# Kernel optimization log

Hardware: AMD Instinct MI355X
Metric: run time of the kernel (lower is better)

The kernel has to match this reference:

```python
import jax, jax.numpy as jnp
import numpy as np
from jax import lax

H, HH = 512, 256          # hidden_size, per-direction TLSTM hidden
B, S = 16, 4096
NOTE_V, CHUNK_V = 512, 512
NUM_LABELS = 1
STD = 0.02                # initializer_range
LN_EPS = 1e-12


def setup_inputs() -> dict:
    key = jax.random.key(0)
    ks = jax.random.split(key, 12)
    n = lambda k, s: jax.random.normal(k, s, jnp.float32) * STD
    return {
        "inputs": jax.random.normal(ks[0], (B, S, H), jnp.float32),
        "times": jax.random.uniform(ks[1], (B, S, 1), jnp.float32),
        "new_note_ids": jax.random.randint(ks[2], (B, S), 0, NOTE_V),
        "new_chunk_ids": jax.random.randint(ks[3], (B, S), 0, CHUNK_V),
        "note_emb": n(ks[4], (NOTE_V, H)),
        "chunk_emb": n(ks[5], (CHUNK_V, H)),
        "W_comb": n(ks[6], (3 * H, H)),
        "b_comb": jnp.zeros((H,), jnp.float32),
        "ln_g": jnp.ones((H,), jnp.float32),
        "ln_b": jnp.zeros((H,), jnp.float32),
        "Wx": n(ks[7], (2, 4, H, HH)),    # [dir, gate(i,f,o,c), in, hid]
        "Wh": n(ks[8], (2, 4, HH, HH)),
        "bg": jnp.zeros((2, 4, HH), jnp.float32),
        "Wd": n(ks[9], (2, HH, HH)),      # W_decomp per direction
        "bd": jnp.zeros((2, HH), jnp.float32),
        "W_cls": n(ks[10], (H, NUM_LABELS)),
        "b_cls": jnp.zeros((NUM_LABELS,), jnp.float32),
    }


def _run_dir(xseq, tseq, Wx, Wh, bg, Wd, bd):
    # xseq: [S,B,H], tseq: [S,B,1]
    def step(carry, xt):
        h, c = carry
        x, t = xt
        T = 1.0 / jnp.log(t + jnp.e)                  # time decay, [B,1] -> broadcast [B,HH]
        c_st = jnp.tanh(c @ Wd + bd)                  # short-term memory
        c_adj = c - c_st + T * c_st                   # discounted cell
        g = jax.nn.sigmoid(jnp.einsum('bd,kdh->kbh', x, Wx)
                           + jnp.einsum('bh,kho->kbo', h, Wh)
                           + bg[:, None, :])          # note: candidate uses sigmoid in original
        i, f, o, cg = g[0], g[1], g[2], g[3]
        ct = f * c_adj + i * cg
        hn = o * jnp.tanh(ct)
        return (hn, ct), hn
    z = jnp.zeros((xseq.shape[1], Wh.shape[-1]), xseq.dtype)
    _, hs = lax.scan(step, (z, z), (xseq, tseq))
    return hs  # [S,B,HH]


def reference(inputs, times, new_note_ids, new_chunk_ids, note_emb, chunk_emb,
              W_comb, b_comb, ln_g, ln_b, Wx, Wh, bg, Wd, bd, W_cls, b_cls):
    # PatientLevelEmbedding (embed_mode='all'), dropout = identity (eval)
    x = jnp.concatenate([inputs, note_emb[new_note_ids], chunk_emb[new_chunk_ids]],
                        axis=-1) @ W_comb + b_comb
    mu = jnp.mean(x, -1, keepdims=True)
    var = jnp.mean((x - mu) ** 2, -1, keepdims=True)
    x = (x - mu) / jnp.sqrt(var + LN_EPS) * ln_g + ln_b

    xs = jnp.transpose(x, (1, 0, 2))      # [S,B,H]  (batch_first permute)
    ts = jnp.transpose(times, (1, 0, 2))  # [S,B,1]

    hs_f = _run_dir(xs, ts, Wx[0], Wh[0], bg[0], Wd[0], bd[0])
    # backward pass: time at step 0 is times[0], then flipped times shifted by one
    t_bwd = jnp.concatenate([ts[:1], jnp.flip(ts, 0)[:-1]], axis=0)
    hs_b = _run_dir(jnp.flip(xs, 0), t_bwd, Wx[1], Wh[1], bg[1], Wd[1], bd[1])

    hidden = jnp.concatenate([hs_f, hs_b], axis=-1)   # [S,B,2*HH]
    drop_in = hidden[-1, 0, :]                        # == lstm_output[0, -1, :] batch-first
    logits = drop_in @ W_cls + b_cls
    logits = jnp.where(jnp.isnan(logits) | jnp.isinf(logits), 0.0, logits)
    pred = jax.nn.sigmoid(logits)
    pred = jnp.where(jnp.isnan(pred) | jnp.isinf(pred), 0.0, pred)
    return pred
```

## Files before the change

### kernel.cpp

```cpp
#include <hip/hip_runtime.h>
#include <math.h>

#define SQ 4096
#define HD 512
#define HHD 256
#define TS 8

#define BAR_LDS() asm volatile("s_waitcnt lgkmcnt(0)\n\ts_barrier" ::: "memory")

typedef _Float16 h2 __attribute__((ext_vector_type(2)));

__device__ __forceinline__ h2 u2h(unsigned v) { union { unsigned u; h2 h; } x; x.u = v; return x.h; }
__device__ __forceinline__ unsigned h2u(h2 v) { union { unsigned u; h2 h; } x; x.h = v; return x.u; }

__device__ __forceinline__ float fdot2f(h2 a, h2 b, float c) {
#if __has_builtin(__builtin_amdgcn_fdot2)
  return __builtin_amdgcn_fdot2(a, b, c, false);
#else
  return fmaf((float)a.x, (float)b.x, fmaf((float)a.y, (float)b.y, c));
#endif
}

__global__ __launch_bounds__(512) void kA(const float* __restrict__ inputs,
                                          const int* __restrict__ nid,
                                          const int* __restrict__ cid,
                                          const float* __restrict__ note_emb,
                                          const float* __restrict__ chunk_emb,
                                          const float* __restrict__ Wc,
                                          const float* __restrict__ bc,
                                          float* __restrict__ xln) {
  __shared__ float xcat[TS][1536];
  const int t = threadIdx.x;
  const int s0 = blockIdx.x * TS;
  for (int si = 0; si < TS; ++si) {
    const int s = s0 + si;
    xcat[si][t]        = inputs[s * HD + t];
    xcat[si][512 + t]  = note_emb[nid[s] * HD + t];
    xcat[si][1024 + t] = chunk_emb[cid[s] * HD + t];
  }
  __syncthreads();
  float acc[TS];
  const float bcv = bc[t];
#pragma unroll
  for (int si = 0; si < TS; ++si) acc[si] = bcv;
  for (int r = 0; r < 1536; r += 4) {
    const float w0 = Wc[(r + 0) * HD + t];
    const float w1 = Wc[(r + 1) * HD + t];
    const float w2 = Wc[(r + 2) * HD + t];
    const float w3 = Wc[(r + 3) * HD + t];
#pragma unroll
    for (int si = 0; si < TS; ++si) {
      const float4 xv = *reinterpret_cast<const float4*>(&xcat[si][r]);
      acc[si] = fmaf(xv.x, w0, acc[si]);
      acc[si] = fmaf(xv.y, w1, acc[si]);
      acc[si] = fmaf(xv.z, w2, acc[si]);
      acc[si] = fmaf(xv.w, w3, acc[si]);
    }
  }
  for (int si = 0; si < TS; ++si) xln[(s0 + si) * HD + t] = acc[si];
}

__global__ __launch_bounds__(256) void kB(float* __restrict__ xln,
                                          const float* __restrict__ g,
                                          const float* __restrict__ b) {
  __shared__ float red[4];
  __shared__ float mu_s, rs_s;
  const int s = blockIdx.x;
  const int t = threadIdx.x;
  const int wave = t >> 6, lane = t & 63;
  float v0 = xln[s * HD + t];
  float v1 = xln[s * HD + t + 256];
  float sum = v0 + v1;
#pragma unroll
  for (int o = 32; o >= 1; o >>= 1) sum += __shfl_down(sum, o, 64);
  if (lane == 0) red[wave] = sum;
  __syncthreads();
  if (t == 0) mu_s = (red[0] + red[1] + red[2] + red[3]) * (1.0f / 512.0f);
  __syncthreads();
  const float mu = mu_s;
  const float d0 = v0 - mu, d1 = v1 - mu;
  float vs = d0 * d0 + d1 * d1;
#pragma unroll
  for (int o = 32; o >= 1; o >>= 1) vs += __shfl_down(vs, o, 64);
  if (lane == 0) red[wave] = vs;
  __syncthreads();
  if (t == 0) rs_s = rsqrtf((red[0] + red[1] + red[2] + red[3]) * (1.0f / 512.0f) + 1e-12f);
  __syncthreads();
  const float rs = rs_s;
  xln[s * HD + t]       = d0 * rs * g[t] + b[t];
  xln[s * HD + t + 256] = d1 * rs * g[t + 256] + b[t + 256];
}

__global__ __launch_bounds__(512) void kC(const float* __restrict__ xln,
                                          const float* __restrict__ Wx,
                                          const float* __restrict__ bg,
                                          float* __restrict__ gx) {
  __shared__ float xs[TS][HD];
  const int t = threadIdx.x;
  const int dir = blockIdx.y;
  const int s0 = blockIdx.x * TS;
  for (int si = 0; si < TS; ++si) {
    const int sx = dir ? (SQ - 1 - (s0 + si)) : (s0 + si);
    xs[si][t] = xln[sx * HD + t];
  }
  __syncthreads();
  const int k1 = t >> 8, j = t & 255;
  const int k2 = k1 + 2;
  const float* w1 = Wx + (size_t)(dir * 4 + k1) * HD * HHD + j;
  const float* w2 = Wx + (size_t)(dir * 4 + k2) * HD * HHD + j;
  float acc1[TS], acc2[TS];
  const float b1 = bg[(dir * 4 + k1) * HHD + j];
  const float b2 = bg[(dir * 4 + k2) * HHD + j];
#pragma unroll
  for (int si = 0; si < TS; ++si) { acc1[si] = b1; acc2[si] = b2; }
  for (int d = 0; d < HD; d += 4) {
    const float w1a = w1[(d + 0) * HHD], w1b = w1[(d + 1) * HHD];
    const float w1c = w1[(d + 2) * HHD], w1d = w1[(d + 3) * HHD];
    const float w2a = w2[(d + 0) * HHD], w2b = w2[(d + 1) * HHD];
    const float w2c = w2[(d + 2) * HHD], w2d = w2[(d + 3) * HHD];
#pragma unroll
    for (int si = 0; si < TS; ++si) {
      const float4 xv = *reinterpret_cast<const float4*>(&xs[si][d]);
      acc1[si] = fmaf(xv.x, w1a, acc1[si]);
      acc1[si] = fmaf(xv.y, w1b, acc1[si]);
      acc1[si] = fmaf(xv.z, w1c, acc1[si]);
      acc1[si] = fmaf(xv.w, w1d, acc1[si]);
      acc2[si] = fmaf(xv.x, w2a, acc2[si]);
      acc2[si] = fmaf(xv.y, w2b, acc2[si]);
      acc2[si] = fmaf(xv.z, w2c, acc2[si]);
      acc2[si] = fmaf(xv.w, w2d, acc2[si]);
    }
  }
  for (int si = 0; si < TS; ++si) {
    float* row = gx + ((size_t)(dir * SQ + s0 + si)) * 1024;
    row[t]       = acc1[si];
    row[t + 512] = acc2[si];
  }
}

__device__ __forceinline__ float tanh_fast(float x) {
  const float ax = fabsf(x);
  const float e  = __expf(-2.0f * ax);
  const float t  = __fdividef(1.0f - e, 1.0f + e);
  return copysignf(t, x);
}

__global__ __launch_bounds__(512, 2) void kR(const float* __restrict__ gx,
                                             const float* __restrict__ Wh,
                                             const float* __restrict__ Wd,
                                             const float* __restrict__ bd,
                                             const float* __restrict__ times,
                                             unsigned long long* __restrict__ comm,
                                             float* __restrict__ hfin) {
  const int slot = blockIdx.x & 7;
  if (slot >= 2) return;
  const int dir = slot;
  const int wg  = blockIdx.x >> 3;
  const int t   = threadIdx.x;
  const int tt  = t & 127;
  const int sk  = t >> 7;
  const int j   = wg * 128 + tt;
  const int lane = t & 63;

  unsigned long long* mybase = comm + (size_t)((dir * 2 + wg) * 2) * 128;
  const unsigned long long* pbase = comm + (size_t)((dir * 2 + (wg ^ 1)) * 2) * 128;

  h2 wh[128];
#pragma unroll
  for (int i = 0; i < 128; ++i) {
    const int k = i >> 5, p = i & 31;
    const int row = 64 * sk + 2 * p;
    const float w0 = Wh[((size_t)(dir * 4 + k) * HHD + row) * HHD + j];
    const float w1 = Wh[((size_t)(dir * 4 + k) * HHD + row + 1) * HHD + j];
    h2 v; v.x = (_Float16)w0; v.y = (_Float16)w1;
    wh[i] = v;
  }
  h2 wd[32];
#pragma unroll
  for (int i = 0; i < 32; ++i) {
    const int row = 64 * sk + 2 * i;
    const float w0 = Wd[(size_t)dir * HHD * HHD + (size_t)row * HHD + j];
    const float w1 = Wd[(size_t)dir * HHD * HHD + (size_t)(row + 1) * HHD + j];
    h2 v; v.x = (_Float16)w0; v.y = (_Float16)w1;
    wd[i] = v;
  }

  __shared__ unsigned h16[128];
  __shared__ unsigned c16[128];
  __shared__ float pg[4][4][128];
  __shared__ float pd[4][128];
  __shared__ float T_pre[SQ];

  for (int s = t; s < SQ; s += 512) {
    const int sidx = dir ? ((s == 0) ? 0 : (SQ - s)) : s;
    T_pre[s] = 1.0f / logf(times[sidx] + 2.7182818284590452354f);
  }
  if (t < 128) { h16[t] = 0u; c16[t] = 0u; }
  __syncthreads();

  const float bdv = (t < 128) ? bd[dir * HHD + j] : 0.0f;
  const float* gxd = gx + (size_t)dir * SQ * 1024 + j;
  float g0 = 0, g1 = 0, g2 = 0, g3 = 0;
  if (t < 128) { g0 = gxd[0]; g1 = gxd[256]; g2 = gxd[512]; g3 = gxd[768]; }

  float h_my = 0.0f, c_my = 0.0f;

  for (int s = 0; s < SQ; ++s) {
    float n0 = 0, n1 = 0, n2 = 0, n3 = 0;
    if (t < 128 && s + 1 < SQ) {
      const float* row = gxd + (size_t)(s + 1) * 1024;
      n0 = row[0]; n1 = row[256]; n2 = row[512]; n3 = row[768];
    }
    float a0 = 0, a1 = 0, a2 = 0, a3 = 0, ad = 0;
    const int base = 32 * sk;
#pragma unroll
    for (int i = 0; i < 32; ++i) {
      const h2 hp = u2h(h16[base + i]);
      a0 = fdot2f(wh[i],       hp, a0);
      a1 = fdot2f(wh[32 + i],  hp, a1);
      a2 = fdot2f(wh[64 + i],  hp, a2);
      a3 = fdot2f(wh[96 + i],  hp, a3);
      const h2 cp = u2h(c16[base + i]);
      ad = fdot2f(wd[i], cp, ad);
    }
    pg[0][sk][tt] = a0;
    pg[1][sk][tt] = a1;
    pg[2][sk][tt] = a2;
    pg[3][sk][tt] = a3;
    pd[sk][tt]    = ad;
    BAR_LDS();
    if (t < 128) {
      const float s0 = pg[0][0][tt] + pg[0][1][tt] + pg[0][2][tt] + pg[0][3][tt];
      const float s1 = pg[1][0][tt] + pg[1][1][tt] + pg[1][2][tt] + pg[1][3][tt];
      const float s2 = pg[2][0][tt] + pg[2][1][tt] + pg[2][2][tt] + pg[2][3][tt];
      const float s3 = pg[3][0][tt] + pg[3][1][tt] + pg[3][2][tt] + pg[3][3][tt];
      const float sd = pd[0][tt] + pd[1][tt] + pd[2][tt] + pd[3][tt];
      const float iv  = __fdividef(1.0f, 1.0f + __expf(-(s0 + g0)));
      const float fv  = __fdividef(1.0f, 1.0f + __expf(-(s1 + g1)));
      const float ov  = __fdividef(1.0f, 1.0f + __expf(-(s2 + g2)));
      const float cgv = __fdividef(1.0f, 1.0f + __expf(-(s3 + g3)));
      const float c_st = tanh_fast(sd + bdv);
      const float T = T_pre[s];
      const float c_adj = c_my + (T - 1.0f) * c_st;
      const float ct = fv * c_adj + iv * cgv;
      const float hn = ov * tanh_fast(ct);
      c_my = ct;
      h_my = hn;
      const float hn_o = __shfl(hn, lane ^ 1, 64);
      const float ct_o = __shfl(ct, lane ^ 1, 64);
      if ((lane & 1) == 0) {
        h2 hp; hp.x = (_Float16)hn; hp.y = (_Float16)hn_o;
        h2 cp; cp.x = (_Float16)ct; cp.y = (_Float16)ct_o;
        const unsigned hu = h2u(hp), cu = h2u(cp);
        const int pl = tt >> 1;
        h16[wg * 64 + pl] = hu;
        c16[wg * 64 + pl] = cu;
        unsigned long long* chunk = (unsigned long long*)mybase + (size_t)(s & 1) * 128;
        const unsigned long long tg = ((unsigned long long)(unsigned)(s + 1)) << 32;
        __hip_atomic_store(chunk + pl,      tg | hu, __ATOMIC_RELAXED, __HIP_MEMORY_SCOPE_AGENT);
        __hip_atomic_store(chunk + 64 + pl, tg | cu, __ATOMIC_RELAXED, __HIP_MEMORY_SCOPE_AGENT);
      }
    } else if (t < 256) {
      const int p = t - 128;
      const unsigned long long* chunk = pbase + (size_t)(s & 1) * 128;
      const unsigned tag = (unsigned)(s + 1);
      unsigned long long v;
      do {
        v = __hip_atomic_load(chunk + p, __ATOMIC_RELAXED, __HIP_MEMORY_SCOPE_AGENT);
      } while ((unsigned)(v >> 32) != tag);
      const unsigned payload = (unsigned)v;
      const int pg_idx = (wg ^ 1) * 64 + (p & 63);
      if (p < 64) h16[pg_idx] = payload;
      else        c16[pg_idx] = payload;
    }
    BAR_LDS();
    g0 = n0; g1 = n1; g2 = n2; g3 = n3;
  }
  if (t < 128) hfin[dir * HHD + j] = h_my;
}

__global__ __launch_bounds__(512) void kD(const float* __restrict__ hfin,
                                          const float* __restrict__ Wcls,
                                          const float* __restrict__ bcls,
                                          float* __restrict__ out) {
  __shared__ float red[8];
  const int t = threadIdx.x;
  float v = hfin[t] * Wcls[t];
#pragma unroll
  for (int o = 32; o >= 1; o >>= 1) v += __shfl_down(v, o, 64);
  if ((t & 63) == 0) red[t >> 6] = v;
  __syncthreads();
  if (t == 0) {
    float l = red[0] + red[1] + red[2] + red[3] + red[4] + red[5] + red[6] + red[7] + bcls[0];
    if (isnan(l) || isinf(l)) l = 0.0f;
    float p = 1.0f / (1.0f + expf(-l));
    if (isnan(p) || isinf(p)) p = 0.0f;
    out[0] = p;
  }
}

extern "C" void kernel_launch(void* const* d_in, const int* in_sizes, int n_in,
                              void* d_out, int out_size, void* d_ws, size_t ws_size,
                              hipStream_t stream) {
  const float* inputs    = (const float*)d_in[0];
  const float* times     = (const float*)d_in[1];
  const int*   nid       = (const int*)d_in[2];
  const int*   cid       = (const int*)d_in[3];
  const float* note_emb  = (const float*)d_in[4];
  const float* chunk_emb = (const float*)d_in[5];
  const float* W_comb    = (const float*)d_in[6];
  const float* b_comb    = (const float*)d_in[7];
  const float* ln_g      = (const float*)d_in[8];
  const float* ln_b      = (const float*)d_in[9];
  const float* Wx        = (const float*)d_in[10];
  const float* Wh        = (const float*)d_in[11];
  const float* bg        = (const float*)d_in[12];
  const float* Wd        = (const float*)d_in[13];
  const float* bd        = (const float*)d_in[14];
  const float* W_cls     = (const float*)d_in[15];
  const float* b_cls     = (const float*)d_in[16];

  float* ws   = (float*)d_ws;
  float* xln  = ws;
  float* gx   = ws + (size_t)SQ * HD;
  float* hfin = gx + (size_t)2 * SQ * 1024;
  unsigned long long* comm = (unsigned long long*)(hfin + 512);

  kA<<<SQ / TS, 512, 0, stream>>>(inputs, nid, cid, note_emb, chunk_emb, W_comb, b_comb, xln);
  kB<<<SQ, 256, 0, stream>>>(xln, ln_g, ln_b);
  kC<<<dim3(SQ / TS, 2), 512, 0, stream>>>(xln, Wx, bg, gx);
  kR<<<10, 512, 0, stream>>>(gx, Wh, Wd, bd, times, comm, hfin);
  kD<<<1, 512, 0, stream>>>(hfin, W_cls, b_cls, (float*)d_out);
}
```

Measured before the change: 7.533 ms.

## Replace second per-step barrier with LDS flag and split own/peer reduction waves

Removes the second workgroup barrier per timestep in the recurrent kernel. The four wave-groups are reassigned so two handle the locally owned half of h/c, which they read from LDS after spinning on a volatile LDS flag. The other two poll the peer workgroup's tagged global slots directly and stage the values into per-wave scratch. Partial-sum buffers are double-buffered by step parity so the next step can start before all readers finish. Loads are vectorised as uint4. The cost is relying on LDS spin-waits and intra-workgroup memory ordering without a barrier, which risks subtle races and wasted cycles from spinning waves.

```diff
diff --git a/kernel.cpp b/kernel.cpp
--- a/kernel.cpp
+++ b/kernel.cpp
@@ -7,6 +7,8 @@
 #define TS 8
 
 #define BAR_LDS() asm volatile("s_waitcnt lgkmcnt(0)\n\ts_barrier" ::: "memory")
+#define FENCE_LDS() asm volatile("s_waitcnt lgkmcnt(0)" ::: "memory")
+#define COMPILER_BARRIER() asm volatile("" ::: "memory")
 
 typedef _Float16 h2 __attribute__((ext_vector_type(2)));
 
@@ -145,6 +147,14 @@
   return copysignf(t, x);
 }
 
+#define DOTQ(hu_, cu_, i_) { \
+  const h2 hp_ = u2h(hu_); \
+  a0 = fdot2f(wh[(i_)],      hp_, a0); \
+  a1 = fdot2f(wh[32 + (i_)], hp_, a1); \
+  a2 = fdot2f(wh[64 + (i_)], hp_, a2); \
+  a3 = fdot2f(wh[96 + (i_)], hp_, a3); \
+  ad = fdot2f(wd[(i_)], u2h(cu_), ad); }
+
 __global__ __launch_bounds__(512, 2) void kR(const float* __restrict__ gx,
                                              const float* __restrict__ Wh,
                                              const float* __restrict__ Wd,
@@ -159,17 +169,21 @@
   const int t   = threadIdx.x;
   const int tt  = t & 127;
   const int sk  = t >> 7;
+  const int skl = sk & 1;
+  const bool own = (sk < 2);
   const int j   = wg * 128 + tt;
   const int lane = t & 63;
 
   unsigned long long* mybase = comm + (size_t)((dir * 2 + wg) * 2) * 128;
   const unsigned long long* pbase = comm + (size_t)((dir * 2 + (wg ^ 1)) * 2) * 128;
 
+  const int basep = (wg ^ (sk >> 1)) * 64 + skl * 32;
+
   h2 wh[128];
 #pragma unroll
   for (int i = 0; i < 128; ++i) {
     const int k = i >> 5, p = i & 31;
-    const int row = 64 * sk + 2 * p;
+    const int row = 2 * (basep + p);
     const float w0 = Wh[((size_t)(dir * 4 + k) * HHD + row) * HHD + j];
     const float w1 = Wh[((size_t)(dir * 4 + k) * HHD + row + 1) * HHD + j];
     h2 v; v.x = (_Float16)w0; v.y = (_Float16)w1;
@@ -178,24 +192,27 @@
   h2 wd[32];
 #pragma unroll
   for (int i = 0; i < 32; ++i) {
-    const int row = 64 * sk + 2 * i;
+    const int row = 2 * (basep + i);
     const float w0 = Wd[(size_t)dir * HHD * HHD + (size_t)row * HHD + j];
     const float w1 = Wd[(size_t)dir * HHD * HHD + (size_t)(row + 1) * HHD + j];
     h2 v; v.x = (_Float16)w0; v.y = (_Float16)w1;
     wd[i] = v;
   }
 
-  __shared__ unsigned h16[128];
-  __shared__ unsigned c16[128];
-  __shared__ float pg[4][4][128];
-  __shared__ float pd[4][128];
+  __shared__ __align__(16) unsigned own_h[64];
+  __shared__ __align__(16) unsigned own_c[64];
+  __shared__ __align__(16) unsigned pscr[2][64];
+  __shared__ float pg[2][4][4][128];
+  __shared__ float pd[2][4][128];
+  __shared__ unsigned hflag[2];
   __shared__ float T_pre[SQ];
 
   for (int s = t; s < SQ; s += 512) {
     const int sidx = dir ? ((s == 0) ? 0 : (SQ - s)) : s;
     T_pre[s] = 1.0f / logf(times[sidx] + 2.7182818284590452354f);
   }
-  if (t < 128) { h16[t] = 0u; c16[t] = 0u; }
+  if (t < 64) { own_h[t] = 0u; own_c[t] = 0u; }
+  if (t == 0) { hflag[0] = 0u; hflag[1] = 0u; }
   __syncthreads();
 
   const float bdv = (t < 128) ? bd[dir * HHD + j] : 0.0f;
@@ -205,36 +222,63 @@
 
   float h_my = 0.0f, c_my = 0.0f;
 
+  const int pslot = (lane < 32) ? (skl * 32 + lane) : (64 + skl * 32 + (lane - 32));
+  volatile unsigned* hf = hflag;
+
   for (int s = 0; s < SQ; ++s) {
+    const int par = s & 1;
     float n0 = 0, n1 = 0, n2 = 0, n3 = 0;
     if (t < 128 && s + 1 < SQ) {
       const float* row = gxd + (size_t)(s + 1) * 1024;
       n0 = row[0]; n1 = row[256]; n2 = row[512]; n3 = row[768];
     }
+
+    const uint4* hp4;
+    const uint4* cp4;
+    if (own) {
+      while (hf[0] != (unsigned)s || hf[1] != (unsigned)s) {}
+      COMPILER_BARRIER();
+      hp4 = (const uint4*)&own_h[skl * 32];
+      cp4 = (const uint4*)&own_c[skl * 32];
+    } else {
+      unsigned pv = 0u;
+      if (s > 0) {
+        const unsigned long long* cptr = pbase + (size_t)((s + 1) & 1) * 128 + pslot;
+        unsigned long long v;
+        do {
+          v = __hip_atomic_load(cptr, __ATOMIC_RELAXED, __HIP_MEMORY_SCOPE_AGENT);
+        } while (__any((int)((unsigned)(v >> 32) != (unsigned)s)));
+        pv = (unsigned)v;
+      }
+      pscr[skl][lane] = pv;
+      FENCE_LDS();
+      hp4 = (const uint4*)&pscr[skl][0];
+      cp4 = (const uint4*)&pscr[skl][32];
+    }
+
     float a0 = 0, a1 = 0, a2 = 0, a3 = 0, ad = 0;
-    const int base = 32 * sk;
-#pragma unroll
-    for (int i = 0; i < 32; ++i) {
-      const h2 hp = u2h(h16[base + i]);
-      a0 = fdot2f(wh[i],       hp, a0);
-      a1 = fdot2f(wh[32 + i],  hp, a1);
-      a2 = fdot2f(wh[64 + i],  hp, a2);
-      a3 = fdot2f(wh[96 + i],  hp, a3);
-      const h2 cp = u2h(c16[base + i]);
-      ad = fdot2f(wd[i], cp, ad);
-    }
-    pg[0][sk][tt] = a0;
-    pg[1][sk][tt] = a1;
-    pg[2][sk][tt] = a2;
-    pg[3][sk][tt] = a3;
-    pd[sk][tt]    = ad;
+#pragma unroll
+    for (int c4 = 0; c4 < 8; ++c4) {
+      const uint4 H = hp4[c4];
+      const uint4 C = cp4[c4];
+      DOTQ(H.x, C.x, 4 * c4 + 0)
+      DOTQ(H.y, C.y, 4 * c4 + 1)
+      DOTQ(H.z, C.z, 4 * c4 + 2)
+      DOTQ(H.w, C.w, 4 * c4 + 3)
+    }
+    pg[par][0][sk][tt] = a0;
+    pg[par][1][sk][tt] = a1;
+    pg[par][2][sk][tt] = a2;
+    pg[par][3][sk][tt] = a3;
+    pd[par][sk][tt]    = ad;
     BAR_LDS();
+
     if (t < 128) {
-      const float s0 = pg[0][0][tt] + pg[0][1][tt] + pg[0][2][tt] + pg[0][3][tt];
-      const float s1 = pg[1][0][tt] + pg[1][1][tt] + pg[1][2][tt] + pg[1][3][tt];
-      const float s2 = pg[2][0][tt] + pg[2][1][tt] + pg[2][2][tt] + pg[2][3][tt];
-      const float s3 = pg[3][0][tt] + pg[3][1][tt] + pg[3][2][tt] + pg[3][3][tt];
-      const float sd = pd[0][tt] + pd[1][tt] + pd[2][tt] + pd[3][tt];
+      const float s0 = pg[par][0][0][tt] + pg[par][0][1][tt] + pg[par][0][2][tt] + pg[par][0][3][tt];
+      const float s1 = pg[par][1][0][tt] + pg[par][1][1][tt] + pg[par][1][2][tt] + pg[par][1][3][tt];
+      const float s2 = pg[par][2][0][tt] + pg[par][2][1][tt] + pg[par][2][2][tt] + pg[par][2][3][tt];
+      const float s3 = pg[par][3][0][tt] + pg[par][3][1][tt] + pg[par][3][2][tt] + pg[par][3][3][tt];
+      const float sd = pd[par][0][tt] + pd[par][1][tt] + pd[par][2][tt] + pd[par][3][tt];
       const float iv  = __fdividef(1.0f, 1.0f + __expf(-(s0 + g0)));
       const float fv  = __fdividef(1.0f, 1.0f + __expf(-(s1 + g1)));
       const float ov  = __fdividef(1.0f, 1.0f + __expf(-(s2 + g2)));
@@ -249,32 +293,22 @@
       const float hn_o = __shfl(hn, lane ^ 1, 64);
       const float ct_o = __shfl(ct, lane ^ 1, 64);
       if ((lane & 1) == 0) {
-        h2 hp; hp.x = (_Float16)hn; hp.y = (_Float16)hn_o;
-        h2 cp; cp.x = (_Float16)ct; cp.y = (_Float16)ct_o;
-        const unsigned hu = h2u(hp), cu = h2u(cp);
+        h2 hp_; hp_.x = (_Float16)hn; hp_.y = (_Float16)hn_o;
+        h2 cp_; cp_.x = (_Float16)ct; cp_.y = (_Float16)ct_o;
+        const unsigned hu = h2u(hp_), cu = h2u(cp_);
         const int pl = tt >> 1;
-        h16[wg * 64 + pl] = hu;
-        c16[wg * 64 + pl] = cu;
-        unsigned long long* chunk = (unsigned long long*)mybase + (size_t)(s & 1) * 128;
+        unsigned long long* chunk = (unsigned long long*)mybase + (size_t)par * 128;
         const unsigned long long tg = ((unsigned long long)(unsigned)(s + 1)) << 32;
         __hip_atomic_store(chunk + pl,      tg | hu, __ATOMIC_RELAXED, __HIP_MEMORY_SCOPE_AGENT);
         __hip_atomic_store(chunk + 64 + pl, tg | cu, __ATOMIC_RELAXED, __HIP_MEMORY_SCOPE_AGENT);
+        own_h[pl] = hu;
+        own_c[pl] = cu;
       }
-    } else if (t < 256) {
-      const int p = t - 128;
-      const unsigned long long* chunk = pbase + (size_t)(s & 1) * 128;
-      const unsigned tag = (unsigned)(s + 1);
-      unsigned long long v;
-      do {
-        v = __hip_atomic_load(chunk + p, __ATOMIC_RELAXED, __HIP_MEMORY_SCOPE_AGENT);
-      } while ((unsigned)(v >> 32) != tag);
-      const unsigned payload = (unsigned)v;
-      const int pg_idx = (wg ^ 1) * 64 + (p & 63);
-      if (p < 64) h16[pg_idx] = payload;
-      else        c16[pg_idx] = payload;
-    }
-    BAR_LDS();
-    g0 = n0; g1 = n1; g2 = n2; g3 = n3;
+      FENCE_LDS();
+      if (t == 0)  hf[0] = (unsigned)(s + 1);
+      if (t == 64) hf[1] = (unsigned)(s + 1);
+      g0 = n0; g1 = n1; g2 = n2; g3 = n3;
+    }
   }
   if (t < 128) hfin[dir * HHD + j] = h_my;
 }
```

Measured after the change: 7.291 ms. -3.2%, faster.
